# Kernel optimization log

Measured on AMD Instinct MI355X. Metric: run time of the kernel, lower is better.

Reference implementation:

```python
import jax, jax.numpy as jnp
import numpy as np

NUM_HEADS = 16
D_MODEL = 1024
HEAD_DIM = D_MODEL // NUM_HEADS
NEG_BIG = 1e10


def setup_inputs() -> dict:
    key = jax.random.key(0)
    k1, k2, k3 = jax.random.split(key, 3)
    B, T = 2, 2048
    from_tensor = jax.random.normal(k1, (B, T, D_MODEL), dtype=jnp.float32)
    init = 0.02
    Wqkv = jax.random.normal(k2, (D_MODEL, 3 * D_MODEL), dtype=jnp.float32) * init
    bqkv = jnp.zeros((3 * D_MODEL,), dtype=jnp.float32)
    Wproj = jax.random.normal(k3, (D_MODEL, D_MODEL), dtype=jnp.float32) * init
    bproj = jnp.zeros((D_MODEL,), dtype=jnp.float32)
    return {"from_tensor": from_tensor, "Wqkv": Wqkv, "bqkv": bqkv,
            "Wproj": Wproj, "bproj": bproj}


def reference(from_tensor, Wqkv, bqkv, Wproj, bproj):
    B, T, D = from_tensor.shape
    H, hd = NUM_HEADS, D // NUM_HEADS
    qkv = from_tensor @ Wqkv + bqkv                      # [B,T,3D]
    q, k, v = jnp.split(qkv, 3, axis=-1)
    def heads(x):  # [B,T,D] -> [B,H,T,hd]
        return x.reshape(B, T, H, hd).transpose(0, 2, 1, 3)
    q, k, v = heads(q), heads(k), heads(v)
    present = jnp.stack([k, v], axis=1)                  # [B,2,H,T,hd]
    scores = jnp.einsum('bhqd,bhkd->bhqk', q, k)         # [B,H,T,T]
    scores = scores * jax.lax.rsqrt(jnp.float32(hd))
    # faithful mask: m = i > j - ns + nd (strict; diagonal masked)
    nd = ns = T
    i = jnp.arange(nd)[:, None]
    j = jnp.arange(ns)
    m = (i > j - ns + nd).astype(scores.dtype)           # [T,T]
    scores = scores * m - NEG_BIG * (1.0 - m)
    probs = jax.nn.softmax(scores, axis=-1)
    ctx = jnp.einsum('bhqk,bhkd->bhqd', probs, v)        # [B,H,T,hd]
    ctx = ctx.transpose(0, 2, 1, 3).reshape(B, T, D)
    out = ctx @ Wproj + bproj                            # [B,T,D]
    return out, present
```

## Files before the change

kernel.cpp:

```cpp
#include <hip/hip_runtime.h>
#include <hip/hip_bf16.h>
#include <cstdint>

typedef __bf16 bf16_t;
typedef __bf16 bf16x4 __attribute__((ext_vector_type(4)));
typedef __bf16 bf16x8 __attribute__((ext_vector_type(8)));
typedef float  f32x4  __attribute__((ext_vector_type(4)));

#define MFMA16(a,b,c) __builtin_amdgcn_mfma_f32_16x16x32_bf16(a,b,c,0,0,0)

#if __has_builtin(__builtin_amdgcn_exp2f)
#define EXP2(x) __builtin_amdgcn_exp2f(x)
#else
#define EXP2(x) exp2f(x)
#endif

__device__ __forceinline__ void gl_lds16(const void* g, void* l){
    __builtin_amdgcn_global_load_lds(
        (const __attribute__((address_space(1))) void*)g,
        (__attribute__((address_space(3))) void*)l, 16, 0, 0);
}

__device__ __forceinline__ void transpose_body(const float* __restrict__ src,
                                               bf16_t* __restrict__ dst,
                                               int R, int C, int c0, int r0,
                                               bf16_t (*tile)[33]){
    int tx = threadIdx.x & 31, g = threadIdx.x >> 5;
#pragma unroll
    for (int p = 0; p < 4; ++p){
        int r = g + p * 8;
        tile[r][tx] = (bf16_t)src[(size_t)(r0 + r) * C + c0 + tx];
    }
    __syncthreads();
#pragma unroll
    for (int p = 0; p < 4; ++p){
        int rr = g + p * 8;
        dst[(size_t)(c0 + rr) * R + r0 + tx] = tile[tx][rr];
    }
}

__global__ void k_prep(const float* __restrict__ X, bf16_t* __restrict__ Xb,
                       const float* __restrict__ Wqkv, bf16_t* __restrict__ WqkvT,
                       const float* __restrict__ Wproj, bf16_t* __restrict__ WprojT){
    __shared__ bf16_t tile[32][33];
    int id = blockIdx.x;
    if (id < 3072){
        int cx = id % 96, cy = id / 96;
        transpose_body(Wqkv, WqkvT, 1024, 3072, cx * 32, cy * 32, tile);
    } else if (id < 4096){
        int t = id - 3072;
        int cx = t & 31, cy = t >> 5;
        transpose_body(Wproj, WprojT, 1024, 1024, cx * 32, cy * 32, tile);
    } else {
        int base = id - 4096;
        for (int i = base * 256 + threadIdx.x; i < 1048576; i += 512 * 256){
            float4 v = ((const float4*)X)[i];
            bf16x4 o = { (bf16_t)v.x, (bf16_t)v.y, (bf16_t)v.z, (bf16_t)v.w };
            ((bf16x4*)Xb)[i] = o;
        }
    }
}

template<int MODE>
__global__ void k_gemm(const bf16_t* __restrict__ A, const bf16_t* __restrict__ Bt,
                       const float* __restrict__ bias,
                       float* __restrict__ Cout,
                       bf16_t* __restrict__ qws, bf16_t* __restrict__ kws,
                       bf16_t* __restrict__ vws,
                       int M, int N, int K){
    __shared__ bf16_t sA[128 * 64];
    __shared__ bf16_t sB[128 * 64];
    int m0 = blockIdx.x * 128, n0 = blockIdx.y * 128;
    int tid = threadIdx.x, lane = tid & 63, w = tid >> 6;
    int lr = lane & 15, lg = lane >> 4;
    int wm = (w >> 1) * 64, wn = (w & 1) * 64;
    f32x4 acc[4][4] = {};

    int srow = lane >> 3;
    int scol = ((lane & 7) ^ srow) * 8;

    for (int k0 = 0; k0 < K; k0 += 64){
#pragma unroll
        for (int p = 0; p < 4; ++p){
            int c = w + p * 4;
            gl_lds16(A  + (size_t)(m0 + c * 8 + srow) * K + k0 + scol, &sA[c * 512]);
            gl_lds16(Bt + (size_t)(n0 + c * 8 + srow) * K + k0 + scol, &sB[c * 512]);
        }
        __syncthreads();
#pragma unroll
        for (int ks = 0; ks < 2; ++ks){
            bf16x8 af[4], bfm[4];
            int ca = ((ks * 4 + lg) ^ (lr & 7)) * 8;
#pragma unroll
            for (int i = 0; i < 4; ++i){
                af[i]  = *(const bf16x8*)(sA + (wm + i * 16 + lr) * 64 + ca);
                bfm[i] = *(const bf16x8*)(sB + (wn + i * 16 + lr) * 64 + ca);
            }
            __builtin_amdgcn_s_setprio(1);
#pragma unroll
            for (int i = 0; i < 4; ++i)
#pragma unroll
                for (int j = 0; j < 4; ++j)
                    acc[i][j] = MFMA16(bfm[j], af[i], acc[i][j]);
            __builtin_amdgcn_s_setprio(0);
        }
        __syncthreads();
    }

#pragma unroll
    for (int j = 0; j < 4; ++j){
        int nb = n0 + wn + j * 16 + lg * 4;
        f32x4 bv = *(const f32x4*)(bias + nb);
#pragma unroll
        for (int i = 0; i < 4; ++i){
            int m = m0 + wm + i * 16 + lr;
            f32x4 cv = acc[i][j];
            cv[0] += bv[0]; cv[1] += bv[1]; cv[2] += bv[2]; cv[3] += bv[3];
            if (MODE == 1){
                *(f32x4*)(Cout + (size_t)m * N + nb) = cv;
            } else {
                int b = m >> 11, t = m & 2047;
                int sec = nb >> 10, rem = nb & 1023;
                int h = rem >> 6, d = rem & 63;
                size_t hbase = (((size_t)b * 16 + h) * 2048 + t) * 64;
                if (sec == 0){
                    bf16x4 qv = {(bf16_t)cv[0], (bf16_t)cv[1], (bf16_t)cv[2], (bf16_t)cv[3]};
                    *(bf16x4*)(qws + hbase + d) = qv;
                } else if (sec == 1){
                    bf16x4 kv = {(bf16_t)cv[0], (bf16_t)cv[1], (bf16_t)cv[2], (bf16_t)cv[3]};
                    *(bf16x4*)(kws + hbase + (d ^ ((t & 7) << 3))) = kv;
                    *(f32x4*)(Cout + ((((size_t)b * 2 + 0) * 16 + h) * 2048 + t) * 64 + d) = cv;
                } else {
                    *(f32x4*)(Cout + ((((size_t)b * 2 + 1) * 16 + h) * 2048 + t) * 64 + d) = cv;
                    int tl = t & 63;
                    int sp = (tl & 0x23) | ((tl & 0x0C) << 1) | ((tl & 0x10) >> 2);
#pragma unroll
                    for (int r = 0; r < 4; ++r){
                        int dd = d + r;
                        vws[(((size_t)b * 16 + h) * 64 + dd) * 2048 + (t & ~63)
                            + (sp ^ ((dd & 7) << 3))] = (bf16_t)cv[r];
                    }
                }
            }
        }
    }
}

__device__ __forceinline__ void stage_kv8(const bf16_t* khead, const bf16_t* vhead,
                                          bf16_t* sKb, bf16_t* sVb,
                                          int kv0, int w, int lane){
    gl_lds16(khead + (size_t)(kv0 + w * 8 + (lane >> 3)) * 64 + (lane & 7) * 8,
             sKb + w * 512);
    gl_lds16(vhead + (size_t)(w * 8 + (lane >> 3)) * 2048 + kv0 + (lane & 7) * 8,
             sVb + w * 512);
}

__global__ __launch_bounds__(512, 4) void k_flash(const bf16_t* __restrict__ qb,
                        const bf16_t* __restrict__ kb, const bf16_t* __restrict__ vt,
                        bf16_t* __restrict__ ctx){
    __shared__ bf16_t sK[3][4096];
    __shared__ bf16_t sV[3][4096];
    int bid = blockIdx.x;
    int x = bid & 7, p = bid >> 3;
    int c = p & 31, pass = p >> 5;
    int bh = x * 4 + pass * 2 + (c >> 4);
    int qt = pass ? 15 - (c & 15) : (c & 15);
    int b = bh >> 4, h = bh & 15;
    int tid = threadIdx.x, lane = tid & 63, w = tid >> 6;
    int lr = lane & 15, lg = lane >> 4;
    int q0 = qt * 128;
    int nkt = 2 * qt + 2;
    const bf16_t* qhead = qb + (size_t)bh * 131072;
    const bf16_t* khead = kb + (size_t)bh * 131072;
    const bf16_t* vhead = vt + (size_t)bh * 131072;
    const float SC = 0.18033688f;

    bf16x8 aq0, aq1;
    {
        const bf16_t* p2 = qhead + (size_t)(q0 + w * 16 + lr) * 64 + lg * 8;
        bf16x8 r0 = *(const bf16x8*)p2, r1 = *(const bf16x8*)(p2 + 32);
#pragma unroll
        for (int j = 0; j < 8; ++j){
            aq0[j] = (bf16_t)((float)r0[j] * SC);
            aq1[j] = (bf16_t)((float)r1[j] * SC);
        }
    }
    float lsum = 0.f;
    f32x4 oacc[4] = {};

    bf16_t *cK = sK[0], *cV = sV[0];
    bf16_t *nK = sK[1], *nV = sV[1];
    bf16_t *xK = sK[2], *xV = sV[2];
    stage_kv8(khead, vhead, cK, cV, 0, w, lane);
    stage_kv8(khead, vhead, nK, nV, 64, w, lane);

    for (int kt = 0; kt < nkt; ++kt){
        asm volatile("s_waitcnt vmcnt(2)" ::: "memory");
        __builtin_amdgcn_s_barrier();
        {
            int nt = kt + 2; if (nt > nkt - 1) nt = nkt - 1;
            stage_kv8(khead, vhead, xK, xV, nt * 64, w, lane);
        }

        bf16x8 kf[8], vf[8];
#pragma unroll
        for (int cf = 0; cf < 4; ++cf){
            kf[cf * 2]     = *(const bf16x8*)(&cK[(cf * 16 + lr) * 64 + ((lg * 8) ^ ((lr & 7) << 3))]);
            kf[cf * 2 + 1] = *(const bf16x8*)(&cK[(cf * 16 + lr) * 64 + ((32 + lg * 8) ^ ((lr & 7) << 3))]);
        }
#pragma unroll
        for (int ks = 0; ks < 2; ++ks)
#pragma unroll
            for (int df = 0; df < 4; ++df)
                vf[ks * 4 + df] = *(const bf16x8*)(&cV[(df * 16 + lr) * 64 + ((ks * 32 + lg * 8) ^ ((lr & 7) << 3))]);

        f32x4 s[4];
        __builtin_amdgcn_s_setprio(1);
#pragma unroll
        for (int cf = 0; cf < 4; ++cf){
            f32x4 a = {};
            a = MFMA16(kf[cf * 2],     aq0, a);
            a = MFMA16(kf[cf * 2 + 1], aq1, a);
            s[cf] = a;
        }
        __builtin_amdgcn_s_setprio(0);
        if (kt >= 2 * qt){
            int qi = q0 + w * 16 + lr;
            int kvg = kt * 64;
#pragma unroll
            for (int cf = 0; cf < 4; ++cf){
                int kvb = kvg + cf * 16 + lg * 4;
#pragma unroll
                for (int r = 0; r < 4; ++r)
                    if (qi <= kvb + r) s[cf][r] = -1e10f;
            }
        }
        __builtin_amdgcn_sched_barrier(0);
        float rsum = 0.f;
        bf16x8 ap0, ap1;
#pragma unroll
        for (int cf = 0; cf < 4; ++cf)
#pragma unroll
            for (int r = 0; r < 4; ++r){
                float pv = EXP2(s[cf][r]);
                rsum += pv;
                if (cf < 2) ap0[(cf & 1) * 4 + r] = (bf16_t)pv;
                else        ap1[(cf & 1) * 4 + r] = (bf16_t)pv;
            }
        lsum += rsum;
        __builtin_amdgcn_s_setprio(1);
#pragma unroll
        for (int ks = 0; ks < 2; ++ks){
            bf16x8 ap = ks ? ap1 : ap0;
#pragma unroll
            for (int df = 0; df < 4; ++df)
                oacc[df] = MFMA16(ap, vf[ks * 4 + df], oacc[df]);
        }
        __builtin_amdgcn_s_setprio(0);
        bf16_t* tK = cK; bf16_t* tV = cV;
        cK = nK; cV = nV; nK = xK; nV = xV; xK = tK; xV = tV;
    }
    asm volatile("s_waitcnt vmcnt(0)" ::: "memory");

    float lt = lsum;
    lt += __shfl_xor(lt, 16);
    lt += __shfl_xor(lt, 32);
    float ls0 = __shfl(lt, lg * 4 + 0);
    float ls1 = __shfl(lt, lg * 4 + 1);
    float ls2 = __shfl(lt, lg * 4 + 2);
    float ls3 = __shfl(lt, lg * 4 + 3);
#pragma unroll
    for (int df = 0; df < 4; ++df){
        int d = df * 16 + lr;
        int tb = q0 + w * 16 + lg * 4;
        size_t base = ((size_t)b * 2048 + tb) * 1024 + h * 64 + d;
        ctx[base]        = (bf16_t)(oacc[df][0] / ls0);
        ctx[base + 1024] = (bf16_t)(oacc[df][1] / ls1);
        ctx[base + 2048] = (bf16_t)(oacc[df][2] / ls2);
        ctx[base + 3072] = (bf16_t)(oacc[df][3] / ls3);
    }
}

__global__ void k_row0fix(const bf16_t* __restrict__ vt, bf16_t* __restrict__ ctx){
    int bh = blockIdx.y;
    int b = bh >> 4, h = bh & 15;
    int lane = threadIdx.x & 63, w = threadIdx.x >> 6;
    int d = blockIdx.x * 4 + w;
    const bf16_t* row = vt + ((size_t)bh * 64 + d) * 2048;
    float s = 0.f;
#pragma unroll
    for (int k = 0; k < 4; ++k){
        bf16x8 v = *(const bf16x8*)(row + (lane + k * 64) * 8);
#pragma unroll
        for (int j = 0; j < 8; ++j) s += (float)v[j];
    }
#pragma unroll
    for (int off = 1; off < 64; off <<= 1) s += __shfl_xor(s, off);
    if (lane == 0)
        ctx[(size_t)b * 2048 * 1024 + h * 64 + d] = (bf16_t)(s * (1.f / 2048.f));
}

extern "C" void kernel_launch(void* const* d_in, const int* in_sizes, int n_in,
                              void* d_out, int out_size, void* d_ws, size_t ws_size,
                              hipStream_t stream){
    const float* X     = (const float*)d_in[0];
    const float* Wqkv  = (const float*)d_in[1];
    const float* bqkv  = (const float*)d_in[2];
    const float* Wproj = (const float*)d_in[3];
    const float* bproj = (const float*)d_in[4];
    float* out = (float*)d_out;
    float* present = out + 4194304;

    char* ws = (char*)d_ws;
    bf16_t* Xb     = (bf16_t*)(ws);
    bf16_t* WqkvT  = (bf16_t*)(ws + 8388608);
    bf16_t* WprojT = (bf16_t*)(ws + 14680064);
    bf16_t* Qb     = (bf16_t*)(ws + 16777216);
    bf16_t* Kb     = (bf16_t*)(ws + 25165824);
    bf16_t* Vt     = (bf16_t*)(ws + 33554432);
    bf16_t* CTXb   = (bf16_t*)(ws + 41943040);

    k_prep<<<4608, 256, 0, stream>>>(X, Xb, Wqkv, WqkvT, Wproj, WprojT);
    k_gemm<0><<<dim3(32, 24), 256, 0, stream>>>(Xb, WqkvT, bqkv, present, Qb, Kb, Vt, 4096, 3072, 1024);
    k_flash<<<512, 512, 0, stream>>>(Qb, Kb, Vt, CTXb);
    k_row0fix<<<dim3(16, 32), 256, 0, stream>>>(Vt, CTXb);
    k_gemm<1><<<dim3(32, 8), 256, 0, stream>>>(CTXb, WprojT, bproj, out, nullptr, nullptr, nullptr, 4096, 1024, 1024);
}
```

Baseline: 96.80 us.

## Double-buffer GEMM LDS tiles with async prefetch over K in steps of 32

Replaces the single 64-wide K tile (load, sync, compute, sync) with two 32-wide LDS buffers. The next-but-one tile is prefetched via global_load_lds while the current one is multiplied, and a vmcnt wait keeps only the newest stage in flight. The aim is to overlap global memory latency with MFMA work in the QKV and projection GEMMs. In exchange it takes more barriers per K step, uses a new swizzle pattern, and issues redundant clamped loads at the tail.

```diff
diff --git a/kernel.cpp b/kernel.cpp
--- a/kernel.cpp
+++ b/kernel.cpp
@@ -68,44 +68,55 @@
                        bf16_t* __restrict__ qws, bf16_t* __restrict__ kws,
                        bf16_t* __restrict__ vws,
                        int M, int N, int K){
-    __shared__ bf16_t sA[128 * 64];
-    __shared__ bf16_t sB[128 * 64];
+    __shared__ bf16_t sA[2][128 * 32];
+    __shared__ bf16_t sB[2][128 * 32];
     int m0 = blockIdx.x * 128, n0 = blockIdx.y * 128;
     int tid = threadIdx.x, lane = tid & 63, w = tid >> 6;
     int lr = lane & 15, lg = lane >> 4;
     int wm = (w >> 1) * 64, wn = (w & 1) * 64;
     f32x4 acc[4][4] = {};
 
-    int srow = lane >> 3;
-    int scol = ((lane & 7) ^ srow) * 8;
-
-    for (int k0 = 0; k0 < K; k0 += 64){
-#pragma unroll
-        for (int p = 0; p < 4; ++p){
+    int srow = lane >> 2;
+    int scol = ((lane & 3) ^ ((lane >> 3) & 3)) * 8;
+
+    auto stage = [&](int bu, int k0){
+#pragma unroll
+        for (int p = 0; p < 2; ++p){
             int c = w + p * 4;
-            gl_lds16(A  + (size_t)(m0 + c * 8 + srow) * K + k0 + scol, &sA[c * 512]);
-            gl_lds16(Bt + (size_t)(n0 + c * 8 + srow) * K + k0 + scol, &sB[c * 512]);
-        }
-        __syncthreads();
-#pragma unroll
-        for (int ks = 0; ks < 2; ++ks){
-            bf16x8 af[4], bfm[4];
-            int ca = ((ks * 4 + lg) ^ (lr & 7)) * 8;
-#pragma unroll
-            for (int i = 0; i < 4; ++i){
-                af[i]  = *(const bf16x8*)(sA + (wm + i * 16 + lr) * 64 + ca);
-                bfm[i] = *(const bf16x8*)(sB + (wn + i * 16 + lr) * 64 + ca);
-            }
-            __builtin_amdgcn_s_setprio(1);
-#pragma unroll
-            for (int i = 0; i < 4; ++i)
-#pragma unroll
-                for (int j = 0; j < 4; ++j)
-                    acc[i][j] = MFMA16(bfm[j], af[i], acc[i][j]);
-            __builtin_amdgcn_s_setprio(0);
-        }
-        __syncthreads();
-    }
+            gl_lds16(A  + (size_t)(m0 + c * 16 + srow) * K + k0 + scol, &sA[bu][c * 512]);
+            gl_lds16(Bt + (size_t)(n0 + c * 16 + srow) * K + k0 + scol, &sB[bu][c * 512]);
+        }
+    };
+
+    int niter = K >> 5;
+    stage(0, 0);
+    stage(1, 32);
+
+    int sw = (lr >> 1) & 3;
+    int ca = ((lg ^ sw)) * 8;
+    for (int kt = 0; kt < niter; ++kt){
+        asm volatile("s_waitcnt vmcnt(4)" ::: "memory");
+        __builtin_amdgcn_s_barrier();
+        const bf16_t* cA = sA[kt & 1];
+        const bf16_t* cB = sB[kt & 1];
+        bf16x8 af[4], bfm[4];
+#pragma unroll
+        for (int i = 0; i < 4; ++i){
+            af[i]  = *(const bf16x8*)(cA + (wm + i * 16 + lr) * 32 + ca);
+            bfm[i] = *(const bf16x8*)(cB + (wn + i * 16 + lr) * 32 + ca);
+        }
+        __builtin_amdgcn_s_setprio(1);
+#pragma unroll
+        for (int i = 0; i < 4; ++i)
+#pragma unroll
+            for (int j = 0; j < 4; ++j)
+                acc[i][j] = MFMA16(bfm[j], af[i], acc[i][j]);
+        __builtin_amdgcn_s_setprio(0);
+        __builtin_amdgcn_s_barrier();
+        int nk = kt + 2; if (nk > niter - 1) nk = niter - 1;
+        stage(kt & 1, nk * 32);
+    }
+    asm volatile("s_waitcnt vmcnt(0)" ::: "memory");
 
 #pragma unroll
     for (int j = 0; j < 4; ++j){
```

Measured after the change: 104.5 us. +7.9%, slower.
